# Performance work log

Hardware: AMD Instinct MI355X
Metric: run time of the kernel (lower is better)

The kernel has to match this reference:

```python
import jax, jax.numpy as jnp
import numpy as np

B, C_IN, H, W = 4, 256, 56, 56
REL, OUT, SP, K, PAD = 16, 256, 8, 7, 3
WS = OUT // SP            # 32 attention-weight channels
K2 = K * K                # 49 window taps
EPS = 1e-5


def _unfold(x, k, pad):
    # reflect-pad (SAN pad_mode=1 -> *_refpad kernels) then gather kxk window taps
    # x: [B,C,H,W] -> [B,C,k*k,H,W], tap order row-major (matches torch Unfold)
    xp = jnp.pad(x, ((0, 0), (0, 0), (pad, pad), (pad, pad)), mode='reflect')
    h, w = x.shape[2], x.shape[3]
    return jnp.stack([xp[:, :, i:i + h, j:j + w]
                      for i in range(k) for j in range(k)], axis=2)


def _conv1x1(x, w, b):
    return jnp.einsum('bchw,oc->bohw', x, w) + b[None, :, None, None]


def _bn(x, g, b, m, v):
    # eval-mode BatchNorm2d over channel axis 1, broadcast over trailing dims
    shape = (1, -1) + (1,) * (x.ndim - 2)
    scale = g.reshape(shape) * jax.lax.rsqrt(v.reshape(shape) + EPS)
    return (x - m.reshape(shape)) * scale + b.reshape(shape)


def _forward(x, w1, b1, w2, b2, w3, b3,
             bn1_g, bn1_b, bn1_m, bn1_v, cw1_w,
             bn2_g, bn2_b, bn2_m, bn2_v, cw2_w, cw2_b, pos2_w):
    x1 = _conv1x1(x, w1, b1)          # [B,REL,H,W]  (query)
    x2 = _conv1x1(x, w2, b2)          # [B,REL,H,W]  (key)
    x3 = _conv1x1(x, w3, b3)          # [B,OUT,H,W]  (value)

    # Subtraction2: q_i - k_j for each of K2 window taps -> [B,REL,K2,H,W]
    diff = x1[:, :, None, :, :] - _unfold(x2, K, PAAD) if False else x1[:, :, None, :, :] - _unfold(x2, K, PAD)

    # conv_w: BN -> ReLU -> 1x1 (no bias) -> BN -> ReLU -> 1x1 (bias)
    h = jax.nn.relu(_bn(diff, bn1_g, bn1_b, bn1_m, bn1_v))
    h = jnp.einsum('bckhw,oc->bokhw', h, cw1_w)
    h = jax.nn.relu(_bn(h, bn2_g, bn2_b, bn2_m, bn2_v))
    h = jnp.einsum('bckhw,oc->bokhw', h, cw2_w) + cw2_b[None, :, None, None, None]
    w = jax.nn.softmax(h, axis=2)     # softmax over K2 taps -> [B,WS,K2,H,W]

    # Aggregation: out[b,c,p] = sum_k unfold(x3)[b,c,k,p] * w[b, c//SP, k, p]
    unf3 = _unfold(x3, K, PAD).reshape(B, WS, SP, K2, H, W)
    agg = jnp.einsum('bgskhw,bgkhw->bgshw', unf3, w).reshape(B, OUT, H, W)

    # use_position2: interleave aggregated values with w, grouped 1x1 conv
    xv = agg.reshape(B, SP, WS, H, W).transpose(0, 2, 1, 3, 4)   # [B,WS,SP,H,W]
    xc = jnp.concatenate([xv, w], axis=2)                        # [B,WS,SP+K2,H,W]
    out = jnp.einsum('bgihw,goi->bgohw', xc, pos2_w).reshape(B, OUT, H, W)
    return out


def setup_inputs() -> dict:
    key = jax.random.key(0)
    ks = jax.random.split(key, 20)
    n = lambda k, s, sc=1.0: jax.random.normal(k, s, dtype=jnp.float32) * sc
    u = lambda k, s: jax.random.uniform(k, s, dtype=jnp.float32, minval=0.5, maxval=1.5)
    return {
        'x': n(ks[0], (B, C_IN, H, W)),
        'w1': n(ks[1], (REL, C_IN), 0.05), 'b1': n(ks[2], (REL,), 0.05),
        'w2': n(ks[3], (REL, C_IN), 0.05), 'b2': n(ks[4], (REL,), 0.05),
        'w3': n(ks[5], (OUT, C_IN), 0.05), 'b3': n(ks[6], (OUT,), 0.05),
        'bn1_g': u(ks[7], (REL,)), 'bn1_b': n(ks[8], (REL,), 0.1),
        'bn1_m': n(ks[9], (REL,), 0.1), 'bn1_v': u(ks[10], (REL,)),
        'cw1_w': n(ks[11], (REL, REL), 0.2),
        'bn2_g': u(ks[12], (REL,)), 'bn2_b': n(ks[13], (REL,), 0.1),
        'bn2_m': n(ks[14], (REL,), 0.1), 'bn2_v': u(ks[15], (REL,)),
        'cw2_w': n(ks[16], (WS, REL), 0.2), 'cw2_b': n(ks[17], (WS,), 0.05),
        'pos2_w': n(ks[18], (WS, SP, SP + K2), 0.1),
    }


def reference(x, w1, b1, w2, b2, w3, b3,
              bn1_g, bn1_b, bn1_m, bn1_v, cw1_w,
              bn2_g, bn2_b, bn2_m, bn2_v, cw2_w, cw2_b, pos2_w):
    return _forward(x, w1, b1, w2, b2, w3, b3,
                    bn1_g, bn1_b, bn1_m, bn1_v, cw1_w,
                    bn2_g, bn2_b, bn2_m, bn2_v, cw2_w, cw2_b, pos2_w)
```

## Files before the change

kernel.cpp:

```cpp
#include <hip/hip_runtime.h>

#define HW 56
#define NPIX 3136
#define CIN 256
#define OUTC 256

typedef unsigned short ushort_t;
typedef unsigned int uint_t;
typedef __attribute__((ext_vector_type(8))) short bf16x8;
typedef __attribute__((ext_vector_type(4))) float f32x4;
typedef __attribute__((ext_vector_type(2))) __fp16 half2v;

__device__ __forceinline__ ushort_t f2b(float f){
  uint_t u = __float_as_uint(f);
  u += 0x7fffu + ((u>>16)&1u);
  return (ushort_t)(u>>16);
}
__device__ __forceinline__ int refl(int v){ v = v<0 ? -v : v; return v>=HW ? 2*HW-2-v : v; }

#define BF_OFF   40960
#define CW1H_OFF 41280
#define CW2H_OFF 41536
#define CW2B_OFF 42048
#define BNC_OFF  42112
#define P2T_OFF  42176
#define X1T_OFF  56768
#define X2T_OFF  257472
#define X3_BYTE_OFF 1832704

__global__ void k0_prep(const float* __restrict__ w1, const float* __restrict__ b1,
                        const float* __restrict__ w2, const float* __restrict__ b2,
                        const float* __restrict__ w3, const float* __restrict__ b3,
                        const float* __restrict__ g1, const float* __restrict__ be1,
                        const float* __restrict__ m1, const float* __restrict__ v1,
                        const float* __restrict__ cw1,
                        const float* __restrict__ g2, const float* __restrict__ be2,
                        const float* __restrict__ m2, const float* __restrict__ v2,
                        const float* __restrict__ cw2, const float* __restrict__ cw2b,
                        const float* __restrict__ p2,
                        float* __restrict__ ws)
{
  int idx = blockIdx.x*256 + threadIdx.x;
  if (idx < 81920){
    int j = idx & 7, l = (idx>>3)&63, t2 = idx>>9;
    int nf = t2 % 20, kt = t2 / 20;
    int k = kt*32 + (l>>4)*8 + j;
    int n = nf*16 + (l&15);
    float v = 0.f;
    if (n < 16)       v = w1[n*256 + k];
    else if (n < 32)  v = w2[(n-16)*256 + k];
    else if (n < 288) v = w3[(n-32)*256 + k];
    ((ushort_t*)ws)[idx] = f2b(v);
    return;
  }
  int j = idx - 81920;
  if (j < 288){ ws[BF_OFF+j] = (j<16 ? b1[j] : (j<32 ? b2[j-16] : b3[j-32])); return; }
  j -= 288;
  if (j < 32){ ws[BF_OFF+288+j] = 0.f; return; }
  j -= 32;
  if (j < 128){
    int o = j>>3, p = j&7;
    union { __fp16 h[2]; uint_t u; } cv;
    cv.h[0] = (__fp16)cw1[o*16 + 2*p];
    cv.h[1] = (__fp16)cw1[o*16 + 2*p+1];
    ((uint_t*)ws)[CW1H_OFF + j] = cv.u;
    return;
  }
  j -= 128;
  if (j < 256){
    int g = j>>3, p = j&7;
    union { __fp16 h[2]; uint_t u; } cv;
    cv.h[0] = (__fp16)cw2[g*16 + 2*p];
    cv.h[1] = (__fp16)cw2[g*16 + 2*p+1];
    ((uint_t*)ws)[CW2H_OFF + j] = cv.u;
    return;
  }
  j -= 256;
  if (j < 32){ ws[CW2B_OFF+j] = cw2b[j]; return; }
  j -= 32;
  if (j < 64){
    int set = j >> 4, c = j & 15;
    float o;
    if (set == 0){ o = g1[c] * rsqrtf(v1[c] + 1e-5f); }
    else if (set == 1){ float s = g1[c] * rsqrtf(v1[c] + 1e-5f); o = be1[c] - m1[c]*s; }
    else if (set == 2){ o = g2[c] * rsqrtf(v2[c] + 1e-5f); }
    else { float s = g2[c] * rsqrtf(v2[c] + 1e-5f); o = be2[c] - m2[c]*s; }
    ws[BNC_OFF+j] = o;
    return;
  }
  j -= 64;
  if (j < 14592){
    int i = j >> 8, rem = j & 255;
    ws[P2T_OFF + j] = p2[rem*57 + i];
    return;
  }
}

__global__ __launch_bounds__(256,2) void k1_proj(const float* __restrict__ x,
                                                 float* __restrict__ ws,
                                                 _Float16* __restrict__ x3h)
{
  __shared__ float xs[CIN*64];
  int t = threadIdx.x;
  int bid = blockIdx.x;
  int b = bid / 49, pp = (bid - b*49)*64;
  int wv = __builtin_amdgcn_readfirstlane(t >> 6);
  int lane = t & 63;

  {
    const float* src = x + (size_t)b*CIN*NPIX + pp;
    int c0 = t >> 4;
    int po = (t & 15) * 4;
    #pragma unroll
    for (int i=0;i<16;i++){
      const float* gp = src + (size_t)(i*16 + c0)*NPIX + po;
      __builtin_amdgcn_global_load_lds(
          (const __attribute__((address_space(1))) void*)gp,
          (__attribute__((address_space(3))) void*)(xs + i*1024 + wv*256),
          16, 0, 0);
    }
  }
  __syncthreads();

  f32x4 acc[4][5];
  float bias[5];
  #pragma unroll
  for (int nf=0;nf<5;nf++) bias[nf] = ws[BF_OFF + wv*80 + nf*16 + (lane&15)];
  #pragma unroll
  for (int m=0;m<4;m++)
    #pragma unroll
    for (int nf=0;nf<5;nf++)
      acc[m][nf] = (f32x4){bias[nf],bias[nf],bias[nf],bias[nf]};

  const uint4* bpk = (const uint4*)ws;
  #pragma unroll 1
  for (int kt=0;kt<8;kt++){
    int abase = (kt*32 + ((lane>>4)<<3))*64 + (lane&15);
    union { uint_t u[4]; bf16x8 v; } ahi[4], alo[4];
    #pragma unroll
    for (int m=0;m<4;m++){
      float f[8];
      #pragma unroll
      for (int j=0;j<8;j++) f[j] = xs[abase + j*64 + m*16];
      #pragma unroll
      for (int p=0;p<4;p++){
        uint_t u0 = __float_as_uint(f[2*p]), u1 = __float_as_uint(f[2*p+1]);
        uint_t h1 = u1 & 0xffff0000u;
        ahi[m].u[p] = (u0>>16) | h1;
        float l0 = f[2*p]   - __uint_as_float(u0 & 0xffff0000u);
        float l1 = f[2*p+1] - __uint_as_float(h1);
        alo[m].u[p] = (__float_as_uint(l0)>>16) | (__float_as_uint(l1) & 0xffff0000u);
      }
    }
    #pragma unroll
    for (int nf=0;nf<5;nf++){
      union { uint4 q; bf16x8 v; } bw;
      bw.q = bpk[(size_t)(kt*20 + wv*5 + nf)*64 + lane];
      #pragma unroll
      for (int m=0;m<4;m++){
        acc[m][nf] = __builtin_amdgcn_mfma_f32_16x16x32_bf16(ahi[m].v, bw.v, acc[m][nf], 0,0,0);
        acc[m][nf] = __builtin_amdgcn_mfma_f32_16x16x32_bf16(alo[m].v, bw.v, acc[m][nf], 0,0,0);
      }
    }
  }

  #pragma unroll
  for (int m=0;m<4;m++){
    #pragma unroll
    for (int r=0;r<4;r++){
      int sp = pp + m*16 + ((lane>>4)<<2) + r;
      #pragma unroll
      for (int nf=0;nf<5;nf++){
        int n = wv*80 + nf*16 + (lane&15);
        float val = acc[m][nf][r];
        if (n < 16){
          ws[X1T_OFF + (size_t)(b*NPIX + sp)*16 + n] = val;
        } else if (n < 32){
          ws[X2T_OFF + (size_t)(b*NPIX + sp)*16 + (n-16)] = val;
        } else if (n < 288){
          x3h[((size_t)b*NPIX + sp)*256 + (n-32)] = (_Float16)val;
        }
      }
    }
  }
}

#define WST 33
__global__ __launch_bounds__(256,5) void k2_fused(const float* __restrict__ ws,
                                                  const _Float16* __restrict__ x3h,
                                                  float* __restrict__ out)
{
  __shared__ float w_s[4*49*WST + 4];
  __shared__ __align__(16) float ags[4*256];

  int tid = threadIdx.x;
  int bid0 = blockIdx.x;
  int bid = (bid0 & 7)*392 + (bid0 >> 3);
  int b = bid / 784; int rem = bid - b*784;
  int row = rem / 14, xs4 = rem - row*14;
  int wv = __builtin_amdgcn_readfirstlane(tid >> 6);
  int lane = tid & 63;
  int y = row, x = xs4*4 + wv;
  int pix = y*HW + x;

  const float* bnc  = ws + BNC_OFF;
  const uint_t* c1h = (const uint_t*)ws + CW1H_OFF;
  const uint_t* c2h = (const uint_t*)ws + CW2H_OFF;
  const float* cw2b = ws + CW2B_OFF;
  float* wp = w_s + wv*49*WST;

  {
    int k = lane;
    int kk = k < 49 ? k : 48;
    int ki = kk / 7, kj = kk - ki*7;
    int gy = refl(y + ki - 3), gx = refl(x + kj - 3);
    int go = gy*HW + gx;

    const float*  x1p = ws + X1T_OFF + (size_t)(b*NPIX + pix)*16;
    const float4* x2p = (const float4*)(ws + X2T_OFF + (size_t)(b*NPIX + go)*16);
    float4 v0 = x2p[0], v1 = x2p[1], v2 = x2p[2], v3 = x2p[3];
    float x2v[16] = {v0.x,v0.y,v0.z,v0.w, v1.x,v1.y,v1.z,v1.w,
                     v2.x,v2.y,v2.z,v2.w, v3.x,v3.y,v3.z,v3.w};
    float h1[16];
    #pragma unroll
    for (int c=0;c<16;c++){
      float d = x1p[c] - x2v[c];
      h1[c] = fmaxf(d*bnc[c] + bnc[16+c], 0.f);
    }
    half2v hp[8];
    #pragma unroll
    for (int p=0;p<8;p++) hp[p] = __builtin_amdgcn_cvt_pkrtz(h1[2*p], h1[2*p+1]);

    float tt[16];
    #pragma unroll
    for (int o=0;o<16;o++){
      float a = 0.f;
      #pragma unroll
      for (int p=0;p<8;p++){
        union { uint_t u; half2v h; } cv; cv.u = c1h[o*8+p];
        a = __builtin_amdgcn_fdot2(hp[p], cv.h, a, false);
      }
      tt[o] = fmaxf(a*bnc[32+o] + bnc[48+o], 0.f);
    }
    half2v tp[8];
    #pragma unroll
    for (int p=0;p<8;p++) tp[p] = __builtin_amdgcn_cvt_pkrtz(tt[2*p], tt[2*p+1]);

    if (k < 49){
      #pragma unroll
      for (int g=0;g<32;g++){
        float a = cw2b[g];
        #pragma unroll
        for (int p=0;p<8;p++){
          union { uint_t u; half2v h; } cv; cv.u = c2h[g*8+p];
          a = __builtin_amdgcn_fdot2(tp[p], cv.h, a, false);
        }
        wp[k*WST + g] = a;
      }
    }
  }

  {
    int half = lane >> 5, g = lane & 31;
    float e[25];
    float M = -3.0e38f;
    #pragma unroll
    for (int i=0;i<25;i++){
      if (half == 0 || i < 24){
        e[i] = wp[(half*25 + i)*WST + g];
        M = fmaxf(M, e[i]);
      }
    }
    M = fmaxf(M, __shfl_xor(M, 32, 64));
    float s = 0.f;
    #pragma unroll
    for (int i=0;i<25;i++){
      if (half == 0 || i < 24){
        e[i] = __expf(e[i] - M);
        s += e[i];
      }
    }
    s += __shfl_xor(s, 32, 64);
    float inv = 1.f / s;
    #pragma unroll
    for (int i=0;i<25;i++){
      if (half == 0 || i < 24) wp[(half*25 + i)*WST + g] = e[i] * inv;
    }
  }

  {
    int g_ = lane >> 1;
    int c0 = lane * 4;
    float a0=0.f,a1=0.f,a2=0.f,a3=0.f;
    const _Float16* xb = x3h + (size_t)b*NPIX*256 + c0;
    #pragma unroll
    for (int kt=0;kt<49;kt++){
      int ii = kt/7, jj = kt - ii*7;
      int gy = refl(y + ii - 3), gx = refl(x + jj - 3);
      int gp = gy*HW + gx;
      float wgt = wp[kt*WST + g_];
      union { uint2 u; _Float16 h[4]; } d;
      d.u = *(const uint2*)(xb + (size_t)gp*256);
      a0 += wgt * (float)d.h[0];
      a1 += wgt * (float)d.h[1];
      a2 += wgt * (float)d.h[2];
      a3 += wgt * (float)d.h[3];
    }
    *(float4*)&ags[wv*256 + c0] = make_float4(a0,a1,a2,a3);
  }
  __syncthreads();

  {
    int c = tid, g4 = c >> 3;
    const float* P2 = ws + P2T_OFF;
    float r0=0.f, r1=0.f, r2=0.f, r3=0.f;
    #pragma unroll
    for (int i=0;i<8;i++){
      float pv = P2[i*256 + c];
      r0 += ags[0*256 + i*32 + g4] * pv;
      r1 += ags[1*256 + i*32 + g4] * pv;
      r2 += ags[2*256 + i*32 + g4] * pv;
      r3 += ags[3*256 + i*32 + g4] * pv;
    }
    #pragma unroll 7
    for (int kt=0;kt<49;kt++){
      float pv = P2[(8+kt)*256 + c];
      r0 += w_s[0*49*WST + kt*WST + g4] * pv;
      r1 += w_s[1*49*WST + kt*WST + g4] * pv;
      r2 += w_s[2*49*WST + kt*WST + g4] * pv;
      r3 += w_s[3*49*WST + kt*WST + g4] * pv;
    }
    int pix0 = y*HW + xs4*4;
    *(float4*)(out + ((size_t)(b*256 + c))*NPIX + pix0) = make_float4(r0,r1,r2,r3);
  }
}

extern "C" void kernel_launch(void* const* d_in, const int* in_sizes, int n_in,
                              void* d_out, int out_size, void* d_ws, size_t ws_size,
                              hipStream_t stream) {
  const float* x    = (const float*)d_in[0];
  const float* w1   = (const float*)d_in[1];
  const float* b1   = (const float*)d_in[2];
  const float* w2   = (const float*)d_in[3];
  const float* b2   = (const float*)d_in[4];
  const float* w3   = (const float*)d_in[5];
  const float* b3   = (const float*)d_in[6];
  const float* g1   = (const float*)d_in[7];
  const float* be1  = (const float*)d_in[8];
  const float* m1   = (const float*)d_in[9];
  const float* v1   = (const float*)d_in[10];
  const float* cw1  = (const float*)d_in[11];
  const float* g2   = (const float*)d_in[12];
  const float* be2  = (const float*)d_in[13];
  const float* m2   = (const float*)d_in[14];
  const float* v2   = (const float*)d_in[15];
  const float* cw2  = (const float*)d_in[16];
  const float* cw2b = (const float*)d_in[17];
  const float* p2   = (const float*)d_in[18];

  float* wsf = (float*)d_ws;
  _Float16* x3h = (_Float16*)((char*)d_ws + X3_BYTE_OFF);
  float* o = (float*)d_out;

  k0_prep<<<381, 256, 0, stream>>>(w1,b1,w2,b2,w3,b3,g1,be1,m1,v1,cw1,g2,be2,m2,v2,cw2,cw2b,p2,wsf);
  k1_proj<<<196, 256, 0, stream>>>(x, wsf, x3h);
  k2_fused<<<3136, 256, 0, stream>>>(wsf, x3h, o);
}
```

Baseline: 67.26 us.

## Store attention weights as packed fp16 in LDS and cache tap offsets

The attention logits and softmax weights in k2_fused are now kept in LDS as packed fp16 pairs instead of fp32, which cuts LDS use so launch bounds can rise from 5 to 8 blocks per CU. The weight-only part of the position2 grouped conv now uses fdot2 against a prepacked fp16 copy of pos2_w built in k0_prep. Reflected tap offsets are computed once and cached in shared memory rather than recomputed in the aggregation loop. In exchange, logits and weights lose precision, and the fp16 layout adds extra packing work and cross-lane shuffles.

```diff
diff --git a/kernel.cpp b/kernel.cpp
--- a/kernel.cpp
+++ b/kernel.cpp
@@ -24,9 +24,10 @@
 #define CW2B_OFF 42048
 #define BNC_OFF  42112
 #define P2T_OFF  42176
-#define X1T_OFF  56768
-#define X2T_OFF  257472
-#define X3_BYTE_OFF 1832704
+#define P2H_OFF  56768
+#define X1T_OFF  82368
+#define X2T_OFF  283072
+#define X3_BYTE_OFF 1935104
 
 __global__ void k0_prep(const float* __restrict__ w1, const float* __restrict__ b1,
                         const float* __restrict__ w2, const float* __restrict__ b2,
@@ -94,6 +95,15 @@
     ws[P2T_OFF + j] = p2[rem*57 + i];
     return;
   }
+  j -= 14592;
+  if (j < 25600){
+    int p = j >> 8, c = j & 255;
+    union { __fp16 h[2]; uint_t u; } cv;
+    cv.h[0] = (__fp16)p2[c*57 + 8 + 2*p];
+    cv.h[1] = (2*p+1 < 49) ? (__fp16)p2[c*57 + 9 + 2*p] : (__fp16)0.f;
+    ((uint_t*)ws)[P2H_OFF + j] = cv.u;
+    return;
+  }
 }
 
 __global__ __launch_bounds__(256,2) void k1_proj(const float* __restrict__ x,
@@ -185,12 +195,12 @@
   }
 }
 
-#define WST 33
-__global__ __launch_bounds__(256,5) void k2_fused(const float* __restrict__ ws,
+__global__ __launch_bounds__(256,8) void k2_fused(const float* __restrict__ ws,
                                                   const _Float16* __restrict__ x3h,
                                                   float* __restrict__ out)
 {
-  __shared__ float w_s[4*49*WST + 4];
+  __shared__ uint_t lgw[4*840];
+  __shared__ int    gp_s[4*64];
   __shared__ __align__(16) float ags[4*256];
 
   int tid = threadIdx.x;
@@ -207,7 +217,7 @@
   const uint_t* c1h = (const uint_t*)ws + CW1H_OFF;
   const uint_t* c2h = (const uint_t*)ws + CW2H_OFF;
   const float* cw2b = ws + CW2B_OFF;
-  float* wp = w_s + wv*49*WST;
+  uint_t* wvbase = lgw + wv*840;
 
   {
     int k = lane;
@@ -215,6 +225,7 @@
     int ki = kk / 7, kj = kk - ki*7;
     int gy = refl(y + ki - 3), gx = refl(x + kj - 3);
     int go = gy*HW + gx;
+    gp_s[wv*64 + lane] = go;
 
     const float*  x1p = ws + X1T_OFF + (size_t)(b*NPIX + pix)*16;
     const float4* x2p = (const float4*)(ws + X2T_OFF + (size_t)(b*NPIX + go)*16);
@@ -248,26 +259,34 @@
 
     if (k < 49){
       #pragma unroll
-      for (int g=0;g<32;g++){
-        float a = cw2b[g];
+      for (int gp=0; gp<16; gp++){
+        float a0 = cw2b[2*gp], a1 = cw2b[2*gp+1];
         #pragma unroll
         for (int p=0;p<8;p++){
-          union { uint_t u; half2v h; } cv; cv.u = c2h[g*8+p];
-          a = __builtin_amdgcn_fdot2(tp[p], cv.h, a, false);
+          union { uint_t u; half2v h; } e0, e1;
+          e0.u = c2h[(2*gp)*8+p];
+          e1.u = c2h[(2*gp+1)*8+p];
+          a0 = __builtin_amdgcn_fdot2(tp[p], e0.h, a0, false);
+          a1 = __builtin_amdgcn_fdot2(tp[p], e1.h, a1, false);
         }
-        wp[k*WST + g] = a;
+        union { half2v h; uint_t u; } pk;
+        pk.h = __builtin_amdgcn_cvt_pkrtz(a0, a1);
+        wvbase[k*17 + gp] = pk.u;
       }
     }
   }
 
   {
-    int half = lane >> 5, g = lane & 31;
+    int half = lane >> 5, g = lane & 31, gsel = g & 1, gp = g >> 1;
     float e[25];
     float M = -3.0e38f;
     #pragma unroll
     for (int i=0;i<25;i++){
       if (half == 0 || i < 24){
-        e[i] = wp[(half*25 + i)*WST + g];
+        uint_t u = wvbase[(half*25+i)*17 + gp];
+        union { ushort_t s; __fp16 h; } cv;
+        cv.s = gsel ? (ushort_t)(u>>16) : (ushort_t)(u & 0xffffu);
+        e[i] = (float)cv.h;
         M = fmaxf(M, e[i]);
       }
     }
@@ -284,27 +303,52 @@
     float inv = 1.f / s;
     #pragma unroll
     for (int i=0;i<25;i++){
-      if (half == 0 || i < 24) wp[(half*25 + i)*WST + g] = e[i] * inv;
+      if (half == 0 || i < 24) e[i] *= inv;
+    }
+    float other = __shfl_xor(half ? e[0] : e[24], 32, 64);
+    if (half == 0){
+      #pragma unroll
+      for (int p=0;p<12;p++){
+        union { half2v h; uint_t u; } pk;
+        pk.h = __builtin_amdgcn_cvt_pkrtz(e[2*p], e[2*p+1]);
+        wvbase[p*33 + g] = pk.u;
+      }
+      union { half2v h; uint_t u; } pk;
+      pk.h = __builtin_amdgcn_cvt_pkrtz(e[24], other);
+      wvbase[12*33 + g] = pk.u;
+    } else {
+      #pragma unroll
+      for (int q=0;q<11;q++){
+        union { half2v h; uint_t u; } pk;
+        pk.h = __builtin_amdgcn_cvt_pkrtz(e[1+2*q], e[2+2*q]);
+        wvbase[(13+q)*33 + g] = pk.u;
+      }
+      union { half2v h; uint_t u; } pk;
+      pk.h = __builtin_amdgcn_cvt_pkrtz(e[23], 0.f);
+      wvbase[24*33 + g] = pk.u;
     }
   }
 
   {
     int g_ = lane >> 1;
     int c0 = lane * 4;
+    const int* gpp = gp_s + wv*64;
     float a0=0.f,a1=0.f,a2=0.f,a3=0.f;
     const _Float16* xb = x3h + (size_t)b*NPIX*256 + c0;
-    #pragma unroll
-    for (int kt=0;kt<49;kt++){
-      int ii = kt/7, jj = kt - ii*7;
-      int gy = refl(y + ii - 3), gx = refl(x + jj - 3);
-      int gp = gy*HW + gx;
-      float wgt = wp[kt*WST + g_];
-      union { uint2 u; _Float16 h[4]; } d;
-      d.u = *(const uint2*)(xb + (size_t)gp*256);
-      a0 += wgt * (float)d.h[0];
-      a1 += wgt * (float)d.h[1];
-      a2 += wgt * (float)d.h[2];
-      a3 += wgt * (float)d.h[3];
+    #pragma unroll 5
+    for (int p=0;p<25;p++){
+      uint_t wu = wvbase[p*33 + g_];
+      union { ushort_t s; __fp16 h; } wl, wh;
+      wl.s = (ushort_t)(wu & 0xffffu); wh.s = (ushort_t)(wu >> 16);
+      float w0 = (float)wl.h, w1 = (float)wh.h;
+      int gp0 = gpp[2*p], gp1 = gpp[2*p+1];
+      union { uint2 u; _Float16 h[4]; } d0, d1;
+      d0.u = *(const uint2*)(xb + (size_t)gp0*256);
+      d1.u = *(const uint2*)(xb + (size_t)gp1*256);
+      a0 += w0*(float)d0.h[0] + w1*(float)d1.h[0];
+      a1 += w0*(float)d0.h[1] + w1*(float)d1.h[1];
+      a2 += w0*(float)d0.h[2] + w1*(float)d1.h[2];
+      a3 += w0*(float)d0.h[3] + w1*(float)d1.h[3];
     }
     *(float4*)&ags[wv*256 + c0] = make_float4(a0,a1,a2,a3);
   }
@@ -313,6 +357,7 @@
   {
     int c = tid, g4 = c >> 3;
     const float* P2 = ws + P2T_OFF;
+    const uint_t* P2H = (const uint_t*)ws + P2H_OFF;
     float r0=0.f, r1=0.f, r2=0.f, r3=0.f;
     #pragma unroll
     for (int i=0;i<8;i++){
@@ -322,13 +367,18 @@
       r2 += ags[2*256 + i*32 + g4] * pv;
       r3 += ags[3*256 + i*32 + g4] * pv;
     }
-    #pragma unroll 7
-    for (int kt=0;kt<49;kt++){
-      float pv = P2[(8+kt)*256 + c];
-      r0 += w_s[0*49*WST + kt*WST + g4] * pv;
-      r1 += w_s[1*49*WST + kt*WST + g4] * pv;
-      r2 += w_s[2*49*WST + kt*WST + g4] * pv;
-      r3 += w_s[3*49*WST + kt*WST + g4] * pv;
+    #pragma unroll 5
+    for (int p=0;p<25;p++){
+      union { uint_t u; half2v h; } ph; ph.u = P2H[p*256 + c];
+      union { uint_t u; half2v h; } w0, w1, w2, w3;
+      w0.u = lgw[0*840 + p*33 + g4];
+      w1.u = lgw[1*840 + p*33 + g4];
+      w2.u = lgw[2*840 + p*33 + g4];
+      w3.u = lgw[3*840 + p*33 + g4];
+      r0 = __builtin_amdgcn_fdot2(w0.h, ph.h, r0, false);
+      r1 = __builtin_amdgcn_fdot2(w1.h, ph.h, r1, false);
+      r2 = __builtin_amdgcn_fdot2(w2.h, ph.h, r2, false);
+      r3 = __builtin_amdgcn_fdot2(w3.h, ph.h, r3, false);
     }
     int pix0 = y*HW + xs4*4;
     *(float4*)(out + ((size_t)(b*256 + c))*NPIX + pix0) = make_float4(r0,r1,r2,r3);
@@ -362,7 +412,7 @@
   _Float16* x3h = (_Float16*)((char*)d_ws + X3_BYTE_OFF);
   float* o = (float*)d_out;
 
-  k0_prep<<<381, 256, 0, stream>>>(w1,b1,w2,b2,w3,b3,g1,be1,m1,v1,cw1,g2,be2,m2,v2,cw2,cw2b,p2,wsf);
+  k0_prep<<<481, 256, 0, stream>>>(w1,b1,w2,b2,w3,b3,g1,be1,m1,v1,cw1,g2,be2,m2,v2,cw2,cw2b,p2,wsf);
   k1_proj<<<196, 256, 0, stream>>>(x, wsf, x3h);
   k2_fused<<<3136, 256, 0, stream>>>(wsf, x3h, o);
 }
```

After: 64.71 us. -3.8%, faster.
